# Kernel optimization log

Measured on AMD Instinct MI355X. Metric: run time of the kernel, lower is better.

## Reference

```python
import jax, jax.numpy as jnp
import numpy as np

BRIGHT_THRESH = 0.65
SAT_THRESH = 0.15
SMOOTH_K = 15
LAMBDA_L1 = 1.0
LAMBDA_WIN_L1 = 3.0
LAMBDA_WIN_COLOR = 1.0
WINDOW_WEIGHT = 5.0
BASE_WEIGHT = 1.0
TRANSFORM_WEIGHT = 2.0
EPS = 1e-8


def _avg_pool_same(x, k=SMOOTH_K):
    # AvgPool2d(k, stride=1, padding=k//2), count_include_pad=True (torch default)
    p = k // 2
    s = jax.lax.reduce_window(x, 0.0, jax.lax.add, (1, 1, k, k), (1, 1, 1, 1),
                              [(0, 0), (0, 0), (p, p), (p, p)])
    return s / (k * k)


def _window_detector(source):
    # Rescale from [-1,1] to [0,1] if any negative values present
    src = jnp.where(source.min() < 0, (source + 1) * 0.5, source)
    brightness = 0.299 * src[:, 0:1] + 0.587 * src[:, 1:2] + 0.114 * src[:, 2:3]
    bright_mask = jax.nn.sigmoid(20.0 * (brightness - BRIGHT_THRESH))
    saturation = src.max(axis=1, keepdims=True) - src.min(axis=1, keepdims=True)
    low_sat_mask = jax.nn.sigmoid(20.0 * (SAT_THRESH - saturation))
    return _avg_pool_same(bright_mask * low_sat_mask)


def _normalize_ch(x):
    # F.normalize over channel dim with eps clamp
    n = jnp.sqrt(jnp.sum(x * x, axis=1, keepdims=True))
    return x / jnp.maximum(n, EPS)


def setup_inputs() -> dict:
    key = jax.random.key(0)
    k1, k2, k3 = jax.random.split(key, 3)
    shape = (16, 3, 512, 512)
    return {
        "pred": jax.random.normal(k1, shape, dtype=jnp.float32),
        "target": jax.random.normal(k2, shape, dtype=jnp.float32),
        "source": jax.random.normal(k3, shape, dtype=jnp.float32),
    }


def reference(pred, target, source):
    window_mask = _window_detector(source)  # [B,1,H,W]

    # plain L1
    l1_loss = jnp.abs(pred - target).mean()

    # window-weighted L1
    weight_map = BASE_WEIGHT + (WINDOW_WEIGHT - BASE_WEIGHT) * window_mask
    win_l1_loss = (jnp.abs(pred - target) * weight_map).mean()

    # window color-transform loss
    st = target - source  # source -> target direction
    sp = pred - source    # source -> pred direction
    alignment = jnp.sum(_normalize_ch(st) * _normalize_ch(sp), axis=1, keepdims=True)
    st_mag = jnp.sqrt(jnp.sum(st * st, axis=1, keepdims=True))
    sp_mag = jnp.sqrt(jnp.sum(sp * sp, axis=1, keepdims=True))
    mag_loss = jnp.abs(sp_mag / (st_mag + EPS) - 1.0)
    color_loss = TRANSFORM_WEIGHT * (window_mask * (1.0 - alignment + 0.5 * mag_loss)).mean()

    total = LAMBDA_L1 * l1_loss + LAMBDA_WIN_L1 * win_l1_loss + LAMBDA_WIN_COLOR * color_loss
    return total
```

## Files before the change

### kernel.cpp

```cpp
#include <hip/hip_runtime.h>
#include <math.h>

#define W 512
#define H 512
#define BATCH 16
#define HW (W * H)
#define NPIX (BATCH * HW)
#define NELEM (3 * NPIX)

#define TW 64
#define TH 32
#define TILES_X (W / TW)
#define TILES_Y (H / TH)
#define TILES_PER_IMG (TILES_X * TILES_Y)
#define NBLOCKS (BATCH * TILES_PER_IMG)

#define MROWS (TH + 14)
#define MCOLS (TW + 14)
#define MSTRIDE 81
#define HSTRIDE 68

__global__ __launch_bounds__(256, 4) void k_fused(const float* __restrict__ pred,
                                                  const float* __restrict__ targ,
                                                  const float* __restrict__ srcp,
                                                  float* __restrict__ partials) {
    __shared__ float smask[MROWS * MSTRIDE];
    __shared__ __align__(16) float shsum[MROWS * HSTRIDE];

    const int tid = threadIdx.x;
    const int bid = blockIdx.x;
    const int b  = bid >> 7;
    const int tl = bid & 127;
    const int ty = tl >> 3;
    const int tx = tl & 7;
    const int y0 = ty * TH;
    const int x0 = tx * TW;
    const size_t ibase = (size_t)b * 3 * HW;

    for (int idx = tid; idx < MROWS * MCOLS; idx += 256) {
        const int row = idx / MCOLS;
        const int col = idx - row * MCOLS;
        const int gy = y0 - 7 + row;
        const int gx = x0 - 7 + col;
        float mval = 0.f;
        if ((unsigned)gy < (unsigned)H && (unsigned)gx < (unsigned)W) {
            const size_t o = ibase + (size_t)gy * W + gx;
            const float R = (srcp[o]          + 1.f) * 0.5f;
            const float G = (srcp[o + HW]     + 1.f) * 0.5f;
            const float B = (srcp[o + 2 * HW] + 1.f) * 0.5f;
            const float bright = 0.299f * R + 0.587f * G + 0.114f * B;
            const float sat = fmaxf(R, fmaxf(G, B)) - fminf(R, fminf(G, B));
            const float bm = 1.f / (1.f + __expf(-20.f * (bright - 0.65f)));
            const float sm = 1.f / (1.f + __expf(-20.f * (0.15f - sat)));
            mval = bm * sm;
        }
        smask[row * MSTRIDE + col] = mval;
    }
    __syncthreads();

    if (tid < MROWS * 2) {
        const int r = tid >> 1;
        const int h = tid & 1;
        const float* mr = smask + r * MSTRIDE + 32 * h;
        float* hr = shsum + r * HSTRIDE + 32 * h;
        float acc = 0.f;
#pragma unroll
        for (int k = 0; k < 15; ++k) acc += mr[k];
        for (int i = 0; i < 32; ++i) {
            hr[i] = acc;
            if (i < 31) acc += mr[i + 15] - mr[i];
        }
    }
    __syncthreads();

    const int cg = tid & 15;
    const int rg = tid >> 4;
    const int ro0 = 2 * rg;
    const int gx = x0 + 4 * cg;

    float4 S = make_float4(0.f, 0.f, 0.f, 0.f);
#pragma unroll
    for (int k = 0; k < 15; ++k) {
        const float4 hv = *(const float4*)(shsum + (ro0 + k) * HSTRIDE + 4 * cg);
        S.x += hv.x; S.y += hv.y; S.z += hv.z; S.w += hv.w;
    }

    float sA = 0.f, sAW = 0.f, sC = 0.f;
    const float inv225 = 1.f / 225.f;

#pragma unroll
    for (int i = 0; i < 2; ++i) {
        const int ro = ro0 + i;
        if (i == 1) {
            const float4 hadd = *(const float4*)(shsum + (ro0 + 15) * HSTRIDE + 4 * cg);
            const float4 hsub = *(const float4*)(shsum + ro0 * HSTRIDE + 4 * cg);
            S.x += hadd.x - hsub.x; S.y += hadd.y - hsub.y;
            S.z += hadd.z - hsub.z; S.w += hadd.w - hsub.w;
        }
        const float wm[4] = {S.x * inv225, S.y * inv225, S.z * inv225, S.w * inv225};

        const size_t base = ibase + (size_t)(y0 + ro) * W + gx;
        const float4 pR = *(const float4*)(pred + base);
        const float4 pG = *(const float4*)(pred + base + HW);
        const float4 pB = *(const float4*)(pred + base + 2 * HW);
        const float4 tR = *(const float4*)(targ + base);
        const float4 tG = *(const float4*)(targ + base + HW);
        const float4 tB = *(const float4*)(targ + base + 2 * HW);
        const float4 sR = *(const float4*)(srcp + base);
        const float4 sG = *(const float4*)(srcp + base + HW);
        const float4 sB = *(const float4*)(srcp + base + 2 * HW);

        const float pr[4] = {pR.x, pR.y, pR.z, pR.w}, pg[4] = {pG.x, pG.y, pG.z, pG.w},
                    pb[4] = {pB.x, pB.y, pB.z, pB.w};
        const float tr[4] = {tR.x, tR.y, tR.z, tR.w}, tg[4] = {tG.x, tG.y, tG.z, tG.w},
                    tb[4] = {tB.x, tB.y, tB.z, tB.w};
        const float sr[4] = {sR.x, sR.y, sR.z, sR.w}, sg[4] = {sG.x, sG.y, sG.z, sG.w},
                    sb[4] = {sB.x, sB.y, sB.z, sB.w};

#pragma unroll
        for (int j = 0; j < 4; ++j) {
            const float a = fabsf(pr[j] - tr[j]) + fabsf(pg[j] - tg[j]) + fabsf(pb[j] - tb[j]);
            const float stx = tr[j] - sr[j], sty = tg[j] - sg[j], stz = tb[j] - sb[j];
            const float spx = pr[j] - sr[j], spy = pg[j] - sg[j], spz = pb[j] - sb[j];
            const float dot = stx * spx + sty * spy + stz * spz;
            const float stm = sqrtf(stx * stx + sty * sty + stz * stz);
            const float spm = sqrtf(spx * spx + spy * spy + spz * spz);
            const float align = dot / (fmaxf(stm, 1e-8f) * fmaxf(spm, 1e-8f));
            const float mag = fabsf(spm / (stm + 1e-8f) - 1.f);
            const float c = 1.f - align + 0.5f * mag;
            sA  += a;
            sAW += a * wm[j];
            sC  += c * wm[j];
        }
    }

#pragma unroll
    for (int off = 32; off > 0; off >>= 1) {
        sA  += __shfl_down(sA, off);
        sAW += __shfl_down(sAW, off);
        sC  += __shfl_down(sC, off);
    }
    __shared__ float red[3][4];
    const int lane = tid & 63;
    const int wave = tid >> 6;
    if (lane == 0) { red[0][wave] = sA; red[1][wave] = sAW; red[2][wave] = sC; }
    __syncthreads();
    if (tid == 0) {
        partials[(size_t)bid * 3 + 0] = red[0][0] + red[0][1] + red[0][2] + red[0][3];
        partials[(size_t)bid * 3 + 1] = red[1][0] + red[1][1] + red[1][2] + red[1][3];
        partials[(size_t)bid * 3 + 2] = red[2][0] + red[2][1] + red[2][2] + red[2][3];
    }
}

__global__ __launch_bounds__(256) void k_final(const float* __restrict__ partials,
                                               float* __restrict__ out) {
    double a = 0.0, aw = 0.0, c = 0.0;
    for (int i = threadIdx.x; i < NBLOCKS; i += 256) {
        a  += (double)partials[(size_t)i * 3 + 0];
        aw += (double)partials[(size_t)i * 3 + 1];
        c  += (double)partials[(size_t)i * 3 + 2];
    }
#pragma unroll
    for (int off = 32; off > 0; off >>= 1) {
        a  += __shfl_down(a, off);
        aw += __shfl_down(aw, off);
        c  += __shfl_down(c, off);
    }
    __shared__ double rd[3][4];
    const int lane = threadIdx.x & 63;
    const int wave = threadIdx.x >> 6;
    if (lane == 0) { rd[0][wave] = a; rd[1][wave] = aw; rd[2][wave] = c; }
    __syncthreads();
    if (threadIdx.x == 0) {
        const double A  = rd[0][0] + rd[0][1] + rd[0][2] + rd[0][3];
        const double AW = rd[1][0] + rd[1][1] + rd[1][2] + rd[1][3];
        const double C  = rd[2][0] + rd[2][1] + rd[2][2] + rd[2][3];
        const double N = (double)NELEM;
        const double M = (double)NPIX;
        out[0] = (float)((4.0 * A + 12.0 * AW) / N + 2.0 * C / M);
    }
}

extern "C" void kernel_launch(void* const* d_in, const int* in_sizes, int n_in,
                              void* d_out, int out_size, void* d_ws, size_t ws_size,
                              hipStream_t stream) {
    const float* pred = (const float*)d_in[0];
    const float* targ = (const float*)d_in[1];
    const float* src  = (const float*)d_in[2];

    float* partials = (float*)d_ws;

    k_fused<<<NBLOCKS, 256, 0, stream>>>(pred, targ, src, partials);
    k_final<<<1, 256, 0, stream>>>(partials, (float*)d_out);
}
```

Baseline: 173.8 us.

## Replace 2D tile box filter with per-wave vertical strip walk and register ring

Each wavefront now owns an 8-row by 256-column strip and walks down it. It computes the mask row by row, does the horizontal 15-wide sum through a small per-wave LDS buffer, and keeps the vertical running sum in a 15-entry register ring. The old block-wide shared tiles and __syncthreads are gone, and the halo recompute goes from 46x78 per 32x64 tile to 22 rows per 8 rows with a narrow horizontal halo. It also switches sqrt/division to fast AMD intrinsics and writes per-wave partials. Risks are the larger vertical halo relative to the strip height, heavier register use from the ring, and slightly lower precision.

```diff
diff --git a/kernel.cpp b/kernel.cpp
--- a/kernel.cpp
+++ b/kernel.cpp
@@ -8,129 +8,146 @@
 #define NPIX (BATCH * HW)
 #define NELEM (3 * NPIX)
 
-#define TW 64
-#define TH 32
-#define TILES_X (W / TW)
-#define TILES_Y (H / TH)
-#define TILES_PER_IMG (TILES_X * TILES_Y)
-#define NBLOCKS (BATCH * TILES_PER_IMG)
-
-#define MROWS (TH + 14)
-#define MCOLS (TW + 14)
-#define MSTRIDE 81
-#define HSTRIDE 68
-
-__global__ __launch_bounds__(256, 4) void k_fused(const float* __restrict__ pred,
+#define TH 8
+#define NSTRIPS 2048
+#define NBLK 512
+#define NSTEPS 22
+
+__device__ __forceinline__ float fast_rcp(float x)  { return __builtin_amdgcn_rcpf(x); }
+__device__ __forceinline__ float fast_sqrt(float x) { return __builtin_amdgcn_sqrtf(x); }
+
+__device__ __forceinline__ float maskval(float r, float g, float b) {
+    const float R = (r + 1.f) * 0.5f;
+    const float G = (g + 1.f) * 0.5f;
+    const float B = (b + 1.f) * 0.5f;
+    const float bright = 0.299f * R + 0.587f * G + 0.114f * B;
+    const float sat = fmaxf(R, fmaxf(G, B)) - fminf(R, fminf(G, B));
+    const float bm = fast_rcp(1.f + __expf(-20.f * (bright - 0.65f)));
+    const float sm = fast_rcp(1.f + __expf(-20.f * (0.15f - sat)));
+    return bm * sm;
+}
+
+__device__ __forceinline__ float4 maskval4(float4 R4, float4 G4, float4 B4) {
+    float4 m;
+    m.x = maskval(R4.x, G4.x, B4.x);
+    m.y = maskval(R4.y, G4.y, B4.y);
+    m.z = maskval(R4.z, G4.z, B4.z);
+    m.w = maskval(R4.w, G4.w, B4.w);
+    return m;
+}
+
+__global__ __launch_bounds__(256, 2) void k_vwalk(const float* __restrict__ pred,
                                                   const float* __restrict__ targ,
                                                   const float* __restrict__ srcp,
                                                   float* __restrict__ partials) {
-    __shared__ float smask[MROWS * MSTRIDE];
-    __shared__ __align__(16) float shsum[MROWS * HSTRIDE];
-
-    const int tid = threadIdx.x;
-    const int bid = blockIdx.x;
-    const int b  = bid >> 7;
-    const int tl = bid & 127;
-    const int ty = tl >> 3;
-    const int tx = tl & 7;
-    const int y0 = ty * TH;
-    const int x0 = tx * TW;
-    const size_t ibase = (size_t)b * 3 * HW;
-
-    for (int idx = tid; idx < MROWS * MCOLS; idx += 256) {
-        const int row = idx / MCOLS;
-        const int col = idx - row * MCOLS;
-        const int gy = y0 - 7 + row;
-        const int gx = x0 - 7 + col;
-        float mval = 0.f;
-        if ((unsigned)gy < (unsigned)H && (unsigned)gx < (unsigned)W) {
-            const size_t o = ibase + (size_t)gy * W + gx;
-            const float R = (srcp[o]          + 1.f) * 0.5f;
-            const float G = (srcp[o + HW]     + 1.f) * 0.5f;
-            const float B = (srcp[o + 2 * HW] + 1.f) * 0.5f;
-            const float bright = 0.299f * R + 0.587f * G + 0.114f * B;
-            const float sat = fmaxf(R, fmaxf(G, B)) - fminf(R, fminf(G, B));
-            const float bm = 1.f / (1.f + __expf(-20.f * (bright - 0.65f)));
-            const float sm = 1.f / (1.f + __expf(-20.f * (0.15f - sat)));
-            mval = bm * sm;
-        }
-        smask[row * MSTRIDE + col] = mval;
-    }
-    __syncthreads();
-
-    if (tid < MROWS * 2) {
-        const int r = tid >> 1;
-        const int h = tid & 1;
-        const float* mr = smask + r * MSTRIDE + 32 * h;
-        float* hr = shsum + r * HSTRIDE + 32 * h;
-        float acc = 0.f;
-#pragma unroll
-        for (int k = 0; k < 15; ++k) acc += mr[k];
-        for (int i = 0; i < 32; ++i) {
-            hr[i] = acc;
-            if (i < 31) acc += mr[i + 15] - mr[i];
-        }
-    }
-    __syncthreads();
-
-    const int cg = tid & 15;
-    const int rg = tid >> 4;
-    const int ro0 = 2 * rg;
-    const int gx = x0 + 4 * cg;
-
+    __shared__ __align__(16) float lbuf[4 * 2 * 272];
+
+    const int tid  = threadIdx.x;
+    const int wv   = tid >> 6;
+    const int lane = tid & 63;
+    const int sid  = blockIdx.x * 4 + wv;
+    const int img    = sid >> 7;
+    const int s      = sid & 127;
+    const int ystrip = s >> 1;
+    const int xh     = s & 1;
+    const int y0   = ystrip * TH;
+    const int x0q  = xh * 256;
+    const size_t ibase = (size_t)img * 3 * HW;
+    float* wb = lbuf + wv * 544;
+
+    const int  gmx = x0q - 8 + 4 * lane;
+    const bool gmv = (gmx >= 0);
+    const int  ghx = x0q + 248 + 4 * lane;
+    const bool ghv = (lane < 4) && (ghx < W);
+    const int  ex  = x0q + 4 * lane;
+
+    float4 ring[15];
+#pragma unroll
+    for (int k = 0; k < 15; ++k) ring[k] = make_float4(0.f, 0.f, 0.f, 0.f);
     float4 S = make_float4(0.f, 0.f, 0.f, 0.f);
-#pragma unroll
-    for (int k = 0; k < 15; ++k) {
-        const float4 hv = *(const float4*)(shsum + (ro0 + k) * HSTRIDE + 4 * cg);
-        S.x += hv.x; S.y += hv.y; S.z += hv.z; S.w += hv.w;
-    }
-
     float sA = 0.f, sAW = 0.f, sC = 0.f;
     const float inv225 = 1.f / 225.f;
 
 #pragma unroll
-    for (int i = 0; i < 2; ++i) {
-        const int ro = ro0 + i;
-        if (i == 1) {
-            const float4 hadd = *(const float4*)(shsum + (ro0 + 15) * HSTRIDE + 4 * cg);
-            const float4 hsub = *(const float4*)(shsum + ro0 * HSTRIDE + 4 * cg);
-            S.x += hadd.x - hsub.x; S.y += hadd.y - hsub.y;
-            S.z += hadd.z - hsub.z; S.w += hadd.w - hsub.w;
+    for (int i = 0; i < NSTEPS; ++i) {
+        const int yi = y0 - 7 + i;
+        float* buf = wb + (i & 1) * 272;
+        float4 h = make_float4(0.f, 0.f, 0.f, 0.f);
+
+        if (yi >= 0 && yi < H) {
+            float4 mv = make_float4(0.f, 0.f, 0.f, 0.f);
+            if (gmv) {
+                const size_t o = ibase + (size_t)yi * W + gmx;
+                const float4 R4 = *(const float4*)(srcp + o);
+                const float4 G4 = *(const float4*)(srcp + o + HW);
+                const float4 B4 = *(const float4*)(srcp + o + 2 * HW);
+                mv = maskval4(R4, G4, B4);
+            }
+            float4 hv2 = make_float4(0.f, 0.f, 0.f, 0.f);
+            if (ghv) {
+                const size_t o = ibase + (size_t)yi * W + ghx;
+                const float4 R4 = *(const float4*)(srcp + o);
+                const float4 G4 = *(const float4*)(srcp + o + HW);
+                const float4 B4 = *(const float4*)(srcp + o + 2 * HW);
+                hv2 = maskval4(R4, G4, B4);
+            }
+            *(float4*)(buf + 4 * lane) = mv;
+            if (lane < 4) *(float4*)(buf + 256 + 4 * lane) = hv2;
+            __builtin_amdgcn_wave_barrier();
+            const float4 v1 = *(const float4*)(buf + 4 * lane + 4);
+            const float4 v2 = *(const float4*)(buf + 4 * lane + 8);
+            const float4 v3 = *(const float4*)(buf + 4 * lane + 12);
+            const float4 v4 = *(const float4*)(buf + 4 * lane + 16);
+            __builtin_amdgcn_wave_barrier();
+            const float mid = v1.x + v1.y + v1.z + v1.w
+                            + v2.x + v2.y + v2.z + v2.w
+                            + v3.x + v3.y + v3.z + v3.w;
+            h.x = mv.y + mv.z + mv.w + mid;
+            h.y = h.x - mv.y + v4.x;
+            h.z = h.y - mv.z + v4.y;
+            h.w = h.z - mv.w + v4.z;
         }
-        const float wm[4] = {S.x * inv225, S.y * inv225, S.z * inv225, S.w * inv225};
-
-        const size_t base = ibase + (size_t)(y0 + ro) * W + gx;
-        const float4 pR = *(const float4*)(pred + base);
-        const float4 pG = *(const float4*)(pred + base + HW);
-        const float4 pB = *(const float4*)(pred + base + 2 * HW);
-        const float4 tR = *(const float4*)(targ + base);
-        const float4 tG = *(const float4*)(targ + base + HW);
-        const float4 tB = *(const float4*)(targ + base + 2 * HW);
-        const float4 sR = *(const float4*)(srcp + base);
-        const float4 sG = *(const float4*)(srcp + base + HW);
-        const float4 sB = *(const float4*)(srcp + base + 2 * HW);
-
-        const float pr[4] = {pR.x, pR.y, pR.z, pR.w}, pg[4] = {pG.x, pG.y, pG.z, pG.w},
-                    pb[4] = {pB.x, pB.y, pB.z, pB.w};
-        const float tr[4] = {tR.x, tR.y, tR.z, tR.w}, tg[4] = {tG.x, tG.y, tG.z, tG.w},
-                    tb[4] = {tB.x, tB.y, tB.z, tB.w};
-        const float sr[4] = {sR.x, sR.y, sR.z, sR.w}, sg[4] = {sG.x, sG.y, sG.z, sG.w},
-                    sb[4] = {sB.x, sB.y, sB.z, sB.w};
-
-#pragma unroll
-        for (int j = 0; j < 4; ++j) {
-            const float a = fabsf(pr[j] - tr[j]) + fabsf(pg[j] - tg[j]) + fabsf(pb[j] - tb[j]);
-            const float stx = tr[j] - sr[j], sty = tg[j] - sg[j], stz = tb[j] - sb[j];
-            const float spx = pr[j] - sr[j], spy = pg[j] - sg[j], spz = pb[j] - sb[j];
-            const float dot = stx * spx + sty * spy + stz * spz;
-            const float stm = sqrtf(stx * stx + sty * sty + stz * stz);
-            const float spm = sqrtf(spx * spx + spy * spy + spz * spz);
-            const float align = dot / (fmaxf(stm, 1e-8f) * fmaxf(spm, 1e-8f));
-            const float mag = fabsf(spm / (stm + 1e-8f) - 1.f);
-            const float c = 1.f - align + 0.5f * mag;
-            sA  += a;
-            sAW += a * wm[j];
-            sC  += c * wm[j];
+
+        const int ri = i % 15;
+        S.x += h.x - ring[ri].x;  S.y += h.y - ring[ri].y;
+        S.z += h.z - ring[ri].z;  S.w += h.w - ring[ri].w;
+        ring[ri] = h;
+
+        if (i >= 14) {
+            const int r = y0 + i - 14;
+            const float wm[4] = {S.x * inv225, S.y * inv225, S.z * inv225, S.w * inv225};
+            const size_t base = ibase + (size_t)r * W + ex;
+            const float4 pR = *(const float4*)(pred + base);
+            const float4 pG = *(const float4*)(pred + base + HW);
+            const float4 pB = *(const float4*)(pred + base + 2 * HW);
+            const float4 tR = *(const float4*)(targ + base);
+            const float4 tG = *(const float4*)(targ + base + HW);
+            const float4 tB = *(const float4*)(targ + base + 2 * HW);
+            const float4 sR = *(const float4*)(srcp + base);
+            const float4 sG = *(const float4*)(srcp + base + HW);
+            const float4 sB = *(const float4*)(srcp + base + 2 * HW);
+
+            const float pr[4] = {pR.x, pR.y, pR.z, pR.w}, pg[4] = {pG.x, pG.y, pG.z, pG.w},
+                        pb[4] = {pB.x, pB.y, pB.z, pB.w};
+            const float tr[4] = {tR.x, tR.y, tR.z, tR.w}, tg[4] = {tG.x, tG.y, tG.z, tG.w},
+                        tb[4] = {tB.x, tB.y, tB.z, tB.w};
+            const float sr[4] = {sR.x, sR.y, sR.z, sR.w}, sg[4] = {sG.x, sG.y, sG.z, sG.w},
+                        sb[4] = {sB.x, sB.y, sB.z, sB.w};
+#pragma unroll
+            for (int j = 0; j < 4; ++j) {
+                const float a = fabsf(pr[j] - tr[j]) + fabsf(pg[j] - tg[j]) + fabsf(pb[j] - tb[j]);
+                const float stx = tr[j] - sr[j], sty = tg[j] - sg[j], stz = tb[j] - sb[j];
+                const float spx = pr[j] - sr[j], spy = pg[j] - sg[j], spz = pb[j] - sb[j];
+                const float dot = stx * spx + sty * spy + stz * spz;
+                const float stm = fast_sqrt(stx * stx + sty * sty + stz * stz);
+                const float spm = fast_sqrt(spx * spx + spy * spy + spz * spz);
+                const float align = dot * fast_rcp(fmaxf(stm, 1e-8f) * fmaxf(spm, 1e-8f));
+                const float mag = fabsf(spm * fast_rcp(stm + 1e-8f) - 1.f);
+                const float c = 1.f - align + 0.5f * mag;
+                sA  += a;
+                sAW += a * wm[j];
+                sC  += c * wm[j];
+            }
         }
     }
 
@@ -140,22 +157,17 @@
         sAW += __shfl_down(sAW, off);
         sC  += __shfl_down(sC, off);
     }
-    __shared__ float red[3][4];
-    const int lane = tid & 63;
-    const int wave = tid >> 6;
-    if (lane == 0) { red[0][wave] = sA; red[1][wave] = sAW; red[2][wave] = sC; }
-    __syncthreads();
-    if (tid == 0) {
-        partials[(size_t)bid * 3 + 0] = red[0][0] + red[0][1] + red[0][2] + red[0][3];
-        partials[(size_t)bid * 3 + 1] = red[1][0] + red[1][1] + red[1][2] + red[1][3];
-        partials[(size_t)bid * 3 + 2] = red[2][0] + red[2][1] + red[2][2] + red[2][3];
+    if (lane == 0) {
+        partials[(size_t)sid * 3 + 0] = sA;
+        partials[(size_t)sid * 3 + 1] = sAW;
+        partials[(size_t)sid * 3 + 2] = sC;
     }
 }
 
 __global__ __launch_bounds__(256) void k_final(const float* __restrict__ partials,
                                                float* __restrict__ out) {
     double a = 0.0, aw = 0.0, c = 0.0;
-    for (int i = threadIdx.x; i < NBLOCKS; i += 256) {
+    for (int i = threadIdx.x; i < NSTRIPS; i += 256) {
         a  += (double)partials[(size_t)i * 3 + 0];
         aw += (double)partials[(size_t)i * 3 + 1];
         c  += (double)partials[(size_t)i * 3 + 2];
@@ -190,6 +202,6 @@
 
     float* partials = (float*)d_ws;
 
-    k_fused<<<NBLOCKS, 256, 0, stream>>>(pred, targ, src, partials);
+    k_vwalk<<<NBLK, 256, 0, stream>>>(pred, targ, src, partials);
     k_final<<<1, 256, 0, stream>>>(partials, (float*)d_out);
 }
```

After: 245.1 us. +41.1%, slower.
